# Performance work log

Hardware: AMD Instinct MI355X
Metric: run time of the kernel (lower is better)

The kernel has to match this reference:

```python
import jax, jax.numpy as jnp
import numpy as np

NUM_ITEMS = 64
NUM_HIDDEN = 256
BATCH = 1_000_000


def setup_inputs() -> dict:
    key = jax.random.key(0)
    k1, k2, k3 = jax.random.split(key, 3)
    valuations = jax.random.uniform(k1, (BATCH, NUM_ITEMS), dtype=jnp.float32)
    # torch.rand -> uniform [0,1); torch.randn -> normal
    W = jax.random.uniform(k2, (NUM_HIDDEN, NUM_ITEMS), dtype=jnp.float32)
    w0 = jax.random.normal(k3, (NUM_HIDDEN,), dtype=jnp.float32)
    return {"valuations": valuations, "W": W, "w0": w0}


def reference(valuations, W, w0):
    # hidden_outputs uses the *unclamped* W (the torch code clamps W.data after the matmul)
    hidden = jnp.matmul(valuations, W.T) + w0            # [B, H]
    max_hidden = jnp.max(hidden, axis=1)                 # [B]
    max_idx = jnp.argmax(hidden, axis=1)                 # [B]
    utility = jnp.maximum(max_hidden, 0.0)               # [B]
    Wc = jnp.clip(W, 0.0, 1.0)                           # clamp applied to W before gather
    gathered = Wc[max_idx]                               # [B, I] per-sample gather
    alloc = jnp.where((max_hidden > 0.0)[:, None], gathered, 0.0)
    alloc = jnp.clip(alloc, 0.0, 1.0)                    # redundant after Wc clip, kept for fidelity
    payments = jnp.sum(alloc * valuations, axis=1) - utility
    payments = jnp.maximum(payments, 0.0)
    return alloc, payments
```

## Files before the change

### kernel.cpp

```cpp
#include <hip/hip_runtime.h>
#include <cfloat>

#define ITEMS 64
#define HID   256
#define BLK   512
#define WROW  68
#define HROW  72
#define BAND  0.016f
#define MT    2
#define CHUNK 32

typedef __attribute__((ext_vector_type(8))) short bf16x8;
typedef __attribute__((ext_vector_type(4))) float f32x4;

#define MFMA(A,B,C) __builtin_amdgcn_mfma_f32_16x16x32_bf16((A),(B),(C),0,0,0)

__global__ __launch_bounds__(BLK, 2) void rochet_fwd(
    const float* __restrict__ val,
    const float* __restrict__ W,
    const float* __restrict__ w0,
    float* __restrict__ alloc,
    float* __restrict__ pay,
    int batch)
{
    __shared__ __attribute__((aligned(16))) ushort lWh[HID * HROW];
    __shared__ __attribute__((aligned(16))) ushort lWl[HID * HROW];
    __shared__ __attribute__((aligned(16))) float  lWf[HID * WROW];
    __shared__ __attribute__((aligned(16))) ushort cmask[(BLK/2) * 16];
    __shared__ float lw0[HID];
    __shared__ int   stage[BLK / 2];

    const int tid = threadIdx.x;

    {
        const int r  = tid >> 1;
        const int hh = (tid & 1) * 32;
        const float4* wg = reinterpret_cast<const float4*>(W + r * ITEMS + hh);
        float4* wf = reinterpret_cast<float4*>(&lWf[r * WROW + hh]);
        uint*   ph = reinterpret_cast<uint*>(&lWh[r * HROW + hh]);
        uint*   pl = reinterpret_cast<uint*>(&lWl[r * HROW + hh]);
        #pragma unroll
        for (int q = 0; q < 8; ++q) {
            float4 w4 = wg[q];
            wf[q] = w4;
            float f[4] = {w4.x, w4.y, w4.z, w4.w};
            #pragma unroll
            for (int p = 0; p < 2; ++p) {
                uint  b0 = __float_as_uint(f[2*p+0]);
                uint  b1 = __float_as_uint(f[2*p+1]);
                float r0 = f[2*p+0] - __uint_as_float(b0 & 0xffff0000u);
                float r1 = f[2*p+1] - __uint_as_float(b1 & 0xffff0000u);
                ph[2*q+p] = (b0 >> 16) | (b1 & 0xffff0000u);
                pl[2*q+p] = (__float_as_uint(r0) >> 16) | (__float_as_uint(r1) & 0xffff0000u);
            }
        }
        if (tid < HID) lw0[tid] = w0[tid];
    }
    __syncthreads();

    const int wave = tid >> 6, lane = tid & 63;
    const int c = lane & 15, g = lane >> 4;
    const int nchunks = (batch + CHUNK - 1) / CHUNK;
    const int nw = gridDim.x * (BLK / 64);

    for (int ch = blockIdx.x * (BLK / 64) + wave; ch < nchunks; ch += nw) {
        const int ms = ch * CHUNK;

        bf16x8 Ah[MT][2], Al[MT][2];
        #pragma unroll
        for (int m = 0; m < MT; ++m) {
            int srow = ms + m * 16 + c;
            if (srow >= batch) srow = batch - 1;
            const float4* vp = reinterpret_cast<const float4*>(val + (size_t)srow * ITEMS);
            #pragma unroll
            for (int ko = 0; ko < 2; ++ko) {
                float4 fa = vp[ko * 8 + 2 * g + 0];
                float4 fb = vp[ko * 8 + 2 * g + 1];
                float f[8] = {fa.x, fa.y, fa.z, fa.w, fb.x, fb.y, fb.z, fb.w};
                #pragma unroll
                for (int i = 0; i < 8; ++i) {
                    uint  b  = __float_as_uint(f[i]);
                    float rr = f[i] - __uint_as_float(b & 0xffff0000u);
                    Ah[m][ko][i] = (short)(b >> 16);
                    Al[m][ko][i] = (short)(__float_as_uint(rr) >> 16);
                }
            }
        }

        const int tb = c * HROW + g * 8;

        float m1[MT * 4];
        #pragma unroll
        for (int i = 0; i < MT * 4; ++i) m1[i] = -FLT_MAX;

        #pragma unroll
        for (int t = 0; t < 16; ++t) {
            bf16x8 bh0 = *reinterpret_cast<const bf16x8*>(&lWh[tb + t * 16 * HROW]);
            bf16x8 bh1 = *reinterpret_cast<const bf16x8*>(&lWh[tb + t * 16 * HROW + 32]);
            bf16x8 bl0 = *reinterpret_cast<const bf16x8*>(&lWl[tb + t * 16 * HROW]);
            bf16x8 bl1 = *reinterpret_cast<const bf16x8*>(&lWl[tb + t * 16 * HROW + 32]);
            float w0c = lw0[t * 16 + c];
            #pragma unroll
            for (int m = 0; m < MT; ++m) {
                f32x4 a = {0.f, 0.f, 0.f, 0.f};
                a = MFMA(Al[m][0], bh0, a);
                a = MFMA(Ah[m][0], bl0, a);
                a = MFMA(Ah[m][0], bh0, a);
                a = MFMA(Al[m][1], bh1, a);
                a = MFMA(Ah[m][1], bl1, a);
                a = MFMA(Ah[m][1], bh1, a);
                #pragma unroll
                for (int r = 0; r < 4; ++r)
                    m1[m * 4 + r] = fmaxf(m1[m * 4 + r], a[r] + w0c);
            }
        }
        #pragma unroll
        for (int d = 1; d < 16; d <<= 1) {
            #pragma unroll
            for (int i = 0; i < MT * 4; ++i)
                m1[i] = fmaxf(m1[i], __shfl_xor(m1[i], d));
        }
        #pragma unroll
        for (int i = 0; i < MT * 4; ++i) m1[i] -= BAND;

        uint cm[MT * 4];
        #pragma unroll
        for (int i = 0; i < MT * 4; ++i) cm[i] = 0;

        #pragma unroll
        for (int t = 0; t < 16; ++t) {
            bf16x8 bh0 = *reinterpret_cast<const bf16x8*>(&lWh[tb + t * 16 * HROW]);
            bf16x8 bh1 = *reinterpret_cast<const bf16x8*>(&lWh[tb + t * 16 * HROW + 32]);
            bf16x8 bl0 = *reinterpret_cast<const bf16x8*>(&lWl[tb + t * 16 * HROW]);
            bf16x8 bl1 = *reinterpret_cast<const bf16x8*>(&lWl[tb + t * 16 * HROW + 32]);
            float w0c = lw0[t * 16 + c];
            #pragma unroll
            for (int m = 0; m < MT; ++m) {
                f32x4 a = {0.f, 0.f, 0.f, 0.f};
                a = MFMA(Al[m][0], bh0, a);
                a = MFMA(Ah[m][0], bl0, a);
                a = MFMA(Ah[m][0], bh0, a);
                a = MFMA(Al[m][1], bh1, a);
                a = MFMA(Ah[m][1], bl1, a);
                a = MFMA(Ah[m][1], bh1, a);
                #pragma unroll
                for (int r = 0; r < 4; ++r)
                    if (a[r] + w0c >= m1[m * 4 + r]) cm[m * 4 + r] |= (1u << t);
            }
        }
        #pragma unroll
        for (int i = 0; i < MT * 4; ++i)
            cmask[(wave * CHUNK + (i >> 2) * 16 + 4 * g + (i & 3)) * 16 + c] = (ushort)cm[i];
        asm volatile("s_waitcnt lgkmcnt(0)" ::: "memory");

        const int s  = ms + lane;
        const int sc = (s < batch) ? s : (batch - 1);
        const float4* vg = reinterpret_cast<const float4*>(val + (size_t)sc * ITEMS);

        float hbest = -FLT_MAX;
        int   jbest = 0;
        if (lane < CHUNK) {
            const uint* crow = reinterpret_cast<const uint*>(&cmask[(wave * CHUNK + lane) * 16]);
            #pragma unroll
            for (int q = 0; q < 8; ++q) {
                uint e = crow[q];
                while (e) {
                    int b = __ffs(e) - 1;
                    e &= e - 1;
                    int j = ((b & 15) << 4) + 2 * q + (b >> 4);
                    const float4* wr = reinterpret_cast<const float4*>(&lWf[j * WROW]);
                    float aa = 0.0f;
                    #pragma unroll
                    for (int k = 0; k < 16; ++k) {
                        float4 t4 = wr[k];
                        float4 vv = vg[k];
                        aa = fmaf(t4.x, vv.x, aa); aa = fmaf(t4.y, vv.y, aa);
                        aa = fmaf(t4.z, vv.z, aa); aa = fmaf(t4.w, vv.w, aa);
                    }
                    float h = aa + lw0[j];
                    if (h > hbest || (h == hbest && j < jbest)) { hbest = h; jbest = j; }
                }
            }
        }

        const bool pos = hbest > 0.0f;
        if (lane < CHUNK && s < batch) {
            float p = 0.0f;
            const float4* wr = reinterpret_cast<const float4*>(&lWf[jbest * WROW]);
            #pragma unroll
            for (int k = 0; k < 16; ++k) {
                float4 t4 = wr[k];
                float4 vv = vg[k];
                float ox = fminf(fmaxf(t4.x, 0.0f), 1.0f);
                float oy = fminf(fmaxf(t4.y, 0.0f), 1.0f);
                float oz = fminf(fmaxf(t4.z, 0.0f), 1.0f);
                float ow = fminf(fmaxf(t4.w, 0.0f), 1.0f);
                if (!pos) { ox = oy = oz = ow = 0.0f; }
                p = fmaf(ox, vv.x, p);
                p = fmaf(oy, vv.y, p);
                p = fmaf(oz, vv.z, p);
                p = fmaf(ow, vv.w, p);
            }
            p -= fmaxf(hbest, 0.0f);
            pay[s] = fmaxf(p, 0.0f);
        }

        if (lane < CHUNK) stage[wave * CHUNK + lane] = jbest | (pos ? 0x100 : 0);
        asm volatile("s_waitcnt lgkmcnt(0)" ::: "memory");
        float4* allocF4 = reinterpret_cast<float4*>(alloc) + (size_t)ms * (ITEMS / 4);
        #pragma unroll
        for (int k = 0; k < 8; ++k) {
            int f = k * 64 + lane;
            int t = f >> 4, cc = f & 15;
            if (ms + t < batch) {
                int   pk = stage[wave * CHUNK + t];
                int   ti = pk & 0xff;
                bool  tp = (pk & 0x100) != 0;
                float4 wv = *reinterpret_cast<const float4*>(&lWf[ti * WROW + cc * 4]);
                float4 o;
                o.x = tp ? fminf(fmaxf(wv.x, 0.0f), 1.0f) : 0.0f;
                o.y = tp ? fminf(fmaxf(wv.y, 0.0f), 1.0f) : 0.0f;
                o.z = tp ? fminf(fmaxf(wv.z, 0.0f), 1.0f) : 0.0f;
                o.w = tp ? fminf(fmaxf(wv.w, 0.0f), 1.0f) : 0.0f;
                allocF4[f] = o;
            }
        }
    }
}

extern "C" void kernel_launch(void* const* d_in, const int* in_sizes, int n_in,
                              void* d_out, int out_size, void* d_ws, size_t ws_size,
                              hipStream_t stream) {
    const float* val = (const float*)d_in[0];
    const float* W   = (const float*)d_in[1];
    const float* w0  = (const float*)d_in[2];
    float* out = (float*)d_out;
    int batch = in_sizes[0] / ITEMS;
    float* alloc = out;
    float* pay   = out + (size_t)batch * ITEMS;

    int nchunks = (batch + CHUNK - 1) / CHUNK;
    int grid = (nchunks + (BLK / 64) - 1) / (BLK / 64);
    if (grid > 256) grid = 256;
    rochet_fwd<<<grid, BLK, 0, stream>>>(val, W, w0, alloc, pay, batch);
}
```

Before: 523.9 us.

## Cache MFMA results, drop fp32 W smem copy, shrink chunk for occupancy

Keeps the 16 MFMA accumulator tiles in registers so the candidate-mask pass reuses them instead of recomputing the split-bf16 GEMM. The fp32 copy of W in shared memory is dropped and the exact rescoring and alloc writes now read W from global memory (cached in L1/L2). The per-wave chunk shrinks from 32 to 16 rows, and the block grows to 1024 threads with a higher min-blocks launch bound, to raise occupancy. The cost is more register pressure from 16 f32x4 accumulators, global-load latency in the rescoring path, and fewer rows per wave to amortize the W fragment loads.

```diff
diff --git a/kernel.cpp b/kernel.cpp
--- a/kernel.cpp
+++ b/kernel.cpp
@@ -3,19 +3,17 @@
 
 #define ITEMS 64
 #define HID   256
-#define BLK   512
-#define WROW  68
+#define BLK   1024
 #define HROW  72
 #define BAND  0.016f
-#define MT    2
-#define CHUNK 32
+#define CHUNK 16
 
 typedef __attribute__((ext_vector_type(8))) short bf16x8;
 typedef __attribute__((ext_vector_type(4))) float f32x4;
 
 #define MFMA(A,B,C) __builtin_amdgcn_mfma_f32_16x16x32_bf16((A),(B),(C),0,0,0)
 
-__global__ __launch_bounds__(BLK, 2) void rochet_fwd(
+__global__ __launch_bounds__(BLK, 4) void rochet_fwd(
     const float* __restrict__ val,
     const float* __restrict__ W,
     const float* __restrict__ w0,
@@ -25,24 +23,21 @@
 {
     __shared__ __attribute__((aligned(16))) ushort lWh[HID * HROW];
     __shared__ __attribute__((aligned(16))) ushort lWl[HID * HROW];
-    __shared__ __attribute__((aligned(16))) float  lWf[HID * WROW];
-    __shared__ __attribute__((aligned(16))) ushort cmask[(BLK/2) * 16];
+    __shared__ __attribute__((aligned(16))) ushort cmask[(BLK/64) * CHUNK * 16];
     __shared__ float lw0[HID];
-    __shared__ int   stage[BLK / 2];
+    __shared__ int   stage[(BLK/64) * CHUNK];
 
     const int tid = threadIdx.x;
 
     {
-        const int r  = tid >> 1;
-        const int hh = (tid & 1) * 32;
+        const int r  = tid >> 2;
+        const int hh = (tid & 3) * 16;
         const float4* wg = reinterpret_cast<const float4*>(W + r * ITEMS + hh);
-        float4* wf = reinterpret_cast<float4*>(&lWf[r * WROW + hh]);
-        uint*   ph = reinterpret_cast<uint*>(&lWh[r * HROW + hh]);
-        uint*   pl = reinterpret_cast<uint*>(&lWl[r * HROW + hh]);
-        #pragma unroll
-        for (int q = 0; q < 8; ++q) {
+        uint* ph = reinterpret_cast<uint*>(&lWh[r * HROW + hh]);
+        uint* pl = reinterpret_cast<uint*>(&lWl[r * HROW + hh]);
+        #pragma unroll
+        for (int q = 0; q < 4; ++q) {
             float4 w4 = wg[q];
-            wf[q] = w4;
             float f[4] = {w4.x, w4.y, w4.z, w4.w};
             #pragma unroll
             for (int p = 0; p < 2; ++p) {
@@ -62,14 +57,14 @@
     const int c = lane & 15, g = lane >> 4;
     const int nchunks = (batch + CHUNK - 1) / CHUNK;
     const int nw = gridDim.x * (BLK / 64);
+    const int tb = c * HROW + g * 8;
 
     for (int ch = blockIdx.x * (BLK / 64) + wave; ch < nchunks; ch += nw) {
         const int ms = ch * CHUNK;
 
-        bf16x8 Ah[MT][2], Al[MT][2];
-        #pragma unroll
-        for (int m = 0; m < MT; ++m) {
-            int srow = ms + m * 16 + c;
+        bf16x8 Ah[2], Al[2];
+        {
+            int srow = ms + c;
             if (srow >= batch) srow = batch - 1;
             const float4* vp = reinterpret_cast<const float4*>(val + (size_t)srow * ITEMS);
             #pragma unroll
@@ -81,76 +76,58 @@
                 for (int i = 0; i < 8; ++i) {
                     uint  b  = __float_as_uint(f[i]);
                     float rr = f[i] - __uint_as_float(b & 0xffff0000u);
-                    Ah[m][ko][i] = (short)(b >> 16);
-                    Al[m][ko][i] = (short)(__float_as_uint(rr) >> 16);
+                    Ah[ko][i] = (short)(b >> 16);
+                    Al[ko][i] = (short)(__float_as_uint(rr) >> 16);
                 }
             }
         }
 
-        const int tb = c * HROW + g * 8;
-
-        float m1[MT * 4];
-        #pragma unroll
-        for (int i = 0; i < MT * 4; ++i) m1[i] = -FLT_MAX;
-
+        f32x4 acc[16];
         #pragma unroll
         for (int t = 0; t < 16; ++t) {
             bf16x8 bh0 = *reinterpret_cast<const bf16x8*>(&lWh[tb + t * 16 * HROW]);
             bf16x8 bh1 = *reinterpret_cast<const bf16x8*>(&lWh[tb + t * 16 * HROW + 32]);
             bf16x8 bl0 = *reinterpret_cast<const bf16x8*>(&lWl[tb + t * 16 * HROW]);
             bf16x8 bl1 = *reinterpret_cast<const bf16x8*>(&lWl[tb + t * 16 * HROW + 32]);
+            f32x4 a = {0.f, 0.f, 0.f, 0.f};
+            a = MFMA(Al[0], bh0, a);
+            a = MFMA(Ah[0], bl0, a);
+            a = MFMA(Ah[0], bh0, a);
+            a = MFMA(Al[1], bh1, a);
+            a = MFMA(Ah[1], bl1, a);
+            a = MFMA(Ah[1], bh1, a);
+            acc[t] = a;
+        }
+
+        float m1[4] = {-FLT_MAX, -FLT_MAX, -FLT_MAX, -FLT_MAX};
+        #pragma unroll
+        for (int t = 0; t < 16; ++t) {
             float w0c = lw0[t * 16 + c];
             #pragma unroll
-            for (int m = 0; m < MT; ++m) {
-                f32x4 a = {0.f, 0.f, 0.f, 0.f};
-                a = MFMA(Al[m][0], bh0, a);
-                a = MFMA(Ah[m][0], bl0, a);
-                a = MFMA(Ah[m][0], bh0, a);
-                a = MFMA(Al[m][1], bh1, a);
-                a = MFMA(Ah[m][1], bl1, a);
-                a = MFMA(Ah[m][1], bh1, a);
-                #pragma unroll
-                for (int r = 0; r < 4; ++r)
-                    m1[m * 4 + r] = fmaxf(m1[m * 4 + r], a[r] + w0c);
+            for (int r = 0; r < 4; ++r) {
+                acc[t][r] += w0c;
+                m1[r] = fmaxf(m1[r], acc[t][r]);
             }
         }
         #pragma unroll
         for (int d = 1; d < 16; d <<= 1) {
             #pragma unroll
-            for (int i = 0; i < MT * 4; ++i)
-                m1[i] = fmaxf(m1[i], __shfl_xor(m1[i], d));
-        }
-        #pragma unroll
-        for (int i = 0; i < MT * 4; ++i) m1[i] -= BAND;
-
-        uint cm[MT * 4];
-        #pragma unroll
-        for (int i = 0; i < MT * 4; ++i) cm[i] = 0;
-
+            for (int r = 0; r < 4; ++r)
+                m1[r] = fmaxf(m1[r], __shfl_xor(m1[r], d));
+        }
+        #pragma unroll
+        for (int r = 0; r < 4; ++r) m1[r] -= BAND;
+
+        uint cm[4] = {0, 0, 0, 0};
         #pragma unroll
         for (int t = 0; t < 16; ++t) {
-            bf16x8 bh0 = *reinterpret_cast<const bf16x8*>(&lWh[tb + t * 16 * HROW]);
-            bf16x8 bh1 = *reinterpret_cast<const bf16x8*>(&lWh[tb + t * 16 * HROW + 32]);
-            bf16x8 bl0 = *reinterpret_cast<const bf16x8*>(&lWl[tb + t * 16 * HROW]);
-            bf16x8 bl1 = *reinterpret_cast<const bf16x8*>(&lWl[tb + t * 16 * HROW + 32]);
-            float w0c = lw0[t * 16 + c];
-            #pragma unroll
-            for (int m = 0; m < MT; ++m) {
-                f32x4 a = {0.f, 0.f, 0.f, 0.f};
-                a = MFMA(Al[m][0], bh0, a);
-                a = MFMA(Ah[m][0], bl0, a);
-                a = MFMA(Ah[m][0], bh0, a);
-                a = MFMA(Al[m][1], bh1, a);
-                a = MFMA(Ah[m][1], bl1, a);
-                a = MFMA(Ah[m][1], bh1, a);
-                #pragma unroll
-                for (int r = 0; r < 4; ++r)
-                    if (a[r] + w0c >= m1[m * 4 + r]) cm[m * 4 + r] |= (1u << t);
-            }
-        }
-        #pragma unroll
-        for (int i = 0; i < MT * 4; ++i)
-            cmask[(wave * CHUNK + (i >> 2) * 16 + 4 * g + (i & 3)) * 16 + c] = (ushort)cm[i];
+            #pragma unroll
+            for (int r = 0; r < 4; ++r)
+                if (acc[t][r] >= m1[r]) cm[r] |= (1u << t);
+        }
+        #pragma unroll
+        for (int r = 0; r < 4; ++r)
+            cmask[(wave * CHUNK + 4 * g + r) * 16 + c] = (ushort)cm[r];
         asm volatile("s_waitcnt lgkmcnt(0)" ::: "memory");
 
         const int s  = ms + lane;
@@ -168,7 +145,7 @@
                     int b = __ffs(e) - 1;
                     e &= e - 1;
                     int j = ((b & 15) << 4) + 2 * q + (b >> 4);
-                    const float4* wr = reinterpret_cast<const float4*>(&lWf[j * WROW]);
+                    const float4* wr = reinterpret_cast<const float4*>(W + j * ITEMS);
                     float aa = 0.0f;
                     #pragma unroll
                     for (int k = 0; k < 16; ++k) {
@@ -186,7 +163,7 @@
         const bool pos = hbest > 0.0f;
         if (lane < CHUNK && s < batch) {
             float p = 0.0f;
-            const float4* wr = reinterpret_cast<const float4*>(&lWf[jbest * WROW]);
+            const float4* wr = reinterpret_cast<const float4*>(W + jbest * ITEMS);
             #pragma unroll
             for (int k = 0; k < 16; ++k) {
                 float4 t4 = wr[k];
@@ -207,16 +184,17 @@
 
         if (lane < CHUNK) stage[wave * CHUNK + lane] = jbest | (pos ? 0x100 : 0);
         asm volatile("s_waitcnt lgkmcnt(0)" ::: "memory");
+        const float4* Wg4 = reinterpret_cast<const float4*>(W);
         float4* allocF4 = reinterpret_cast<float4*>(alloc) + (size_t)ms * (ITEMS / 4);
         #pragma unroll
-        for (int k = 0; k < 8; ++k) {
+        for (int k = 0; k < 4; ++k) {
             int f = k * 64 + lane;
             int t = f >> 4, cc = f & 15;
             if (ms + t < batch) {
                 int   pk = stage[wave * CHUNK + t];
                 int   ti = pk & 0xff;
                 bool  tp = (pk & 0x100) != 0;
-                float4 wv = *reinterpret_cast<const float4*>(&lWf[ti * WROW + cc * 4]);
+                float4 wv = Wg4[ti * (ITEMS / 4) + cc];
                 float4 o;
                 o.x = tp ? fminf(fmaxf(wv.x, 0.0f), 1.0f) : 0.0f;
                 o.y = tp ? fminf(fmaxf(wv.y, 0.0f), 1.0f) : 0.0f;
```

Result: slower. 959.3 us (+83.1%).
